# Optimization experiments

Hardware: AMD Instinct MI355X
Metric: run time of the kernel (lower is better)

The kernel has to match this reference:

```python
import jax, jax.numpy as jnp
from jax import lax
import numpy as np

B = 262144
CLASSES = 11


def setup_inputs() -> dict:
    key = jax.random.key(0)
    ks = jax.random.split(key, 8)
    exponents = jax.random.randint(ks[0], (B, 16), 0, CLASSES, dtype=jnp.int32)
    conv0_w = jax.random.normal(ks[1], (4, 12, 1, 2), jnp.float32) * 0.1
    conv0_b = jax.random.normal(ks[2], (4,), jnp.float32) * 0.05
    conv1_w = jax.random.normal(ks[3], (4, 12, 2, 1), jnp.float32) * 0.1
    # xavier-uniform linears, bias filled with 0.01 (as in init_weights)
    lim1 = float(np.sqrt(6.0 / (96 + 256)))
    linear_w = jax.random.uniform(ks[4], (256, 96), jnp.float32, -lim1, lim1)
    linear_b = jnp.full((256,), 0.01, jnp.float32)
    lim2 = float(np.sqrt(6.0 / (256 + 4)))
    out_w = jax.random.uniform(ks[5], (4, 256), jnp.float32, -lim2, lim2)
    out_b = jnp.full((4,), 0.01, jnp.float32)
    return {"exponents": exponents, "conv0_w": conv0_w, "conv0_b": conv0_b,
            "conv1_w": conv1_w, "linear_w": linear_w, "linear_b": linear_b,
            "out_w": out_w, "out_b": out_b}


def _conv(x, w):
    return lax.conv_general_dilated(x, w, (1, 1), 'VALID',
                                    dimension_numbers=('NCHW', 'OIHW', 'NCHW'))


def _forward(exponents, conv0_w, conv0_b, conv1_w, linear_w, linear_b, out_w, out_b):
    e = exponents.reshape(-1, 4, 4)
    # reconstruct board values: 0 tile stays 0, else 2**e
    x = jnp.where(e == 0, 0.0, jnp.exp2(e.astype(jnp.float32)))  # [B,4,4]
    # rotate_normalize: flips chosen from argmax corner (computed BEFORE flipping)
    corners = jnp.stack([x[:, 0, 0], x[:, 0, -1], x[:, -1, 0], x[:, -1, -1]], axis=1)
    ix = jnp.argmax(corners, axis=1)
    flip_v = ix >= 2          # floor(ix/2) == 1
    flip_h = (ix % 2) == 1
    x = jnp.where(flip_v[:, None, None], x[:, ::-1, :], x)
    x = jnp.where(flip_h[:, None, None], x[:, :, ::-1], x)
    # log2 with 0 -> 0, one-hot over 11 classes
    x_log = jnp.log2(x + (x == 0).astype(jnp.float32))
    onehot = jax.nn.one_hot(jnp.round(x_log).astype(jnp.int32), CLASSES,
                            dtype=jnp.float32)          # [B,4,4,11]
    onehot = jnp.transpose(onehot, (0, 3, 1, 2))         # [B,11,4,4]
    mask = onehot.sum(axis=1, keepdims=True)             # channel 0 (all ones)
    feat = jnp.concatenate([mask, onehot], axis=1)       # [B,12,4,4]
    zh = jax.nn.relu(_conv(feat, conv0_w) + conv0_b[None, :, None, None])  # [B,4,4,3]
    zv = jax.nn.relu(_conv(feat, conv1_w))                                  # [B,4,3,4]
    z1 = jnp.concatenate([zh.reshape(-1, 48), zv.reshape(-1, 48)], axis=1)  # [B,96]
    z2 = jax.nn.relu(z1 @ linear_w.T + linear_b)                            # [B,256]
    probs = jax.nn.softmax(z2 @ out_w.T + out_b, axis=1)                    # [B,4]
    # unscramble: vert swaps actions (0,1); horiz swaps actions (2,3)
    perm = jnp.stack([jnp.where(flip_v, 1, 0), jnp.where(flip_v, 0, 1),
                      jnp.where(flip_h, 3, 2), jnp.where(flip_h, 2, 3)], axis=1)
    return jnp.take_along_axis(probs, perm, axis=1)


def reference(exponents, conv0_w, conv0_b, conv1_w, linear_w, linear_b, out_w, out_b):
    return _forward(exponents, conv0_w, conv0_b, conv1_w, linear_w, linear_b, out_w, out_b)
```

## Files before the change

kernel.cpp:

```cpp
#include <hip/hip_runtime.h>

typedef unsigned int  u32;
typedef unsigned short u16;

typedef float    f4  __attribute__((ext_vector_type(4)));
typedef short    bf8 __attribute__((ext_vector_type(8)));
typedef __fp16   h8  __attribute__((ext_vector_type(8)));
typedef __fp16   h2  __attribute__((ext_vector_type(2)));

#define NBLK  256
#define ZSTR  104

__device__ __forceinline__ u32 bfr(float f) {
    union { float f; u32 u; } v; v.f = f;
    return (v.u + 0x8000u) >> 16;
}
__device__ __forceinline__ u32 pk2(float lo, float hi) { return bfr(lo) | (bfr(hi) << 16); }
__device__ __forceinline__ u32 pkh(float lo, float hi) {
    union { h2 h; u32 u; } v; v.h = __builtin_amdgcn_cvt_pkrtz(lo, hi); return v.u;
}
__device__ __forceinline__ u32 pkmax0(u32 x) {
    u32 r; asm("v_pk_max_f16 %0, %1, %2" : "=v"(r) : "v"(x), "v"(0u)); return r;
}
__device__ __forceinline__ u32 nrev(u32 x) {
    return ((x >> 12) & 0xFu) | ((x >> 4) & 0xF0u) | ((x << 4) & 0xF00u) | ((x << 12) & 0xF000u);
}
__device__ __forceinline__ void ds_fence() {
    asm volatile("" ::: "memory");
    __builtin_amdgcn_sched_barrier(0);
}

__device__ __forceinline__ void phase1_fn(const int4 e4, u16* __restrict__ zrow,
                                          const uint2* __restrict__ Th, const uint2* __restrict__ Tv,
                                          const int m, const int qd,
                                          bf8& zb0, bf8& zb1, bf8& zb2, bool& fv, bool& fh)
{
    u32 pkd = (u32)e4.x | ((u32)e4.y << 4) | ((u32)e4.z << 8) | ((u32)e4.w << 12);
    u32 R0 = (u32)__shfl((int)pkd, m);
    u32 R1 = (u32)__shfl((int)pkd, m + 16);
    u32 R2 = (u32)__shfl((int)pkd, m + 32);
    u32 R3 = (u32)__shfl((int)pkd, m + 48);
    u32 c0v = R0 & 15u, c1v = (R0 >> 12) & 15u, c2v = R3 & 15u, c3v = (R3 >> 12) & 15u;
    u32 best = c0v; int ix = 0;
    if (c1v > best) { best = c1v; ix = 1; }
    if (c2v > best) { best = c2v; ix = 2; }
    if (c3v > best) { best = c3v; ix = 3; }
    fv = (ix >= 2); fh = ((ix & 1) != 0);
    u32 F0 = fv ? R3 : R0;
    u32 F1 = fv ? R2 : R1;
    u32 F2 = fv ? R1 : R2;
    u32 F3 = fv ? R0 : R3;
    if (fh) { F0 = nrev(F0); F1 = nrev(F1); F2 = nrev(F2); F3 = nrev(F3); }

    const u32 Fq = (qd == 0) ? F0 : (qd == 1) ? F1 : (qd == 2) ? F2 : F3;
    u32 nbq0 = Fq & 15u, nbq1 = (Fq >> 4) & 15u, nbq2 = (Fq >> 8) & 15u, nbq3 = (Fq >> 12) & 15u;
    u32 nbc0 = (F0 >> (4*qd)) & 15u, nbc1 = (F1 >> (4*qd)) & 15u;
    u32 nbc2 = (F2 >> (4*qd)) & 15u, nbc3 = (F3 >> (4*qd)) & 15u;

    uint2 H0 = Th[nbq0*11u + nbq1];
    uint2 H1 = Th[nbq1*11u + nbq2];
    uint2 H2 = Th[nbq2*11u + nbq3];
    uint2 V0 = Tv[nbc0*11u + nbc1];
    uint2 V1 = Tv[nbc1*11u + nbc2];
    uint2 V2 = Tv[nbc2*11u + nbc3];

    *(uint2*)(zrow + (qd*3 + 0)*4) = H0;
    *(uint2*)(zrow + (qd*3 + 1)*4) = H1;
    *(uint2*)(zrow + (qd*3 + 2)*4) = H2;
    *(uint2*)(zrow + 48 + (0*4 + qd)*4) = V0;
    *(uint2*)(zrow + 48 + (1*4 + qd)*4) = V1;
    *(uint2*)(zrow + 48 + (2*4 + qd)*4) = V2;

    ds_fence();

    zb0 = *(const bf8*)(zrow + qd*8);
    zb1 = *(const bf8*)(zrow + 32 + qd*8);
    zb2 = *(const bf8*)(zrow + 64 + qd*8);

    ds_fence();
}

__launch_bounds__(1024, 4)
__global__ void smartcnn_fused(const int* __restrict__ exps,
                               const float* __restrict__ c0w, const float* __restrict__ c0b,
                               const float* __restrict__ c1w,
                               const float* __restrict__ lw,  const float* __restrict__ lb,
                               const float* __restrict__ ow,  const float* __restrict__ ob,
                               float* __restrict__ out)
{
    __shared__ u16   afL[48 * 512];
    __shared__ uint2 ThA[121];
    __shared__ uint2 TvA[121];
    __shared__ f4    lbL[64];
    __shared__ u32   owL[2048];
    __shared__ u16   z1[256 * ZSTR];

    const int tid  = threadIdx.x;
    const int w    = tid >> 6;
    const int lane = tid & 63;
    const int m    = lane & 15;
    const int qd   = lane >> 4;

    if (tid < 242) {
        const int e = (tid < 121) ? tid : tid - 121;
        const int v1 = e / 11, v2 = e - v1*11;
        float a[4];
        #pragma unroll
        for (int c = 0; c < 4; ++c) {
            if (tid < 121)
                a[c] = fmaxf(c0w[c*24 + 0] + c0w[c*24 + (1+v1)*2 + 0] + c0b[c]
                           + c0w[c*24 + 1] + c0w[c*24 + (1+v2)*2 + 1], 0.f);
            else
                a[c] = fmaxf(c1w[c*24 + 0] + c1w[c*24 + (1+v1)*2 + 0]
                           + c1w[c*24 + 1] + c1w[c*24 + (1+v2)*2 + 1], 0.f);
        }
        uint2 v = make_uint2(pk2(a[0], a[1]), pk2(a[2], a[3]));
        if (tid < 121) ThA[tid] = v; else TvA[tid - 121] = v;
    }
    if (tid < 64) {
        const int T = tid >> 2, q = tid & 3;
        const int tb = ((T & 1) ? 4 : 0) + (T >> 1) * 32;
        lbL[tid] = *(const f4*)(lb + tb + 8 * q);
    }
    #pragma unroll
    for (int v = 0; v < 6; ++v) {
        const int x   = v * 4096 + tid * 4;
        const int fid = x / 96;
        const int ko0 = x - fid * 96;
        const int r   = fid & 63;
        const int T   = ((fid >> 6) << 2) | (((r >> 5) & 1) << 1) | ((r >> 2) & 1);
        const int gm  = (((r >> 3) & 3) << 2) | (r & 3);
        const int side = (ko0 >= 48) ? 48 : 0;
        const int kq0  = ko0 - side;
        const int kp0  = side + (kq0 % 12) * 4 + kq0 / 12;
        const int base = T * 1536 + gm * 8;
        const f4 fv4 = *(const f4*)(lw + x);
        #pragma unroll
        for (int e = 0; e < 4; ++e) {
            const int kp  = kp0 + 4 * e;
            const int idx = base + ((kp >> 5) << 9) + (((kp >> 3) & 3) << 7) + (kp & 7);
            afL[idx] = (u16)bfr(fv4[e]);
        }
    }
    if (tid < 512) {
        const int gl = tid & 63, wc = tid >> 6;
        const int gm = gl & 15, gq = gl >> 4;
        const int cc = wc & 1, ww = wc >> 1;
        uint4 v = make_uint4(0u, 0u, 0u, 0u);
        if (gm < 4) {
            const int n8 = 64*ww + 32*cc + gq*8;
            const float* orow = ow + gm*256 + n8;
            v.x = pkh(orow[0], orow[1]);
            v.y = pkh(orow[2], orow[3]);
            v.z = pkh(orow[4], orow[5]);
            v.w = pkh(orow[6], orow[7]);
        }
        *(uint4*)(&owL[tid * 4]) = v;
    }
    const float4 obv = *(const float4*)ob;
    u16* zrow = &z1[(w*16 + m) * ZSTR];

    __syncthreads();

    const int wbase = blockIdx.x * 1024 + w * 64;
    int4 e4a = *(const int4*)(exps + (size_t)(wbase + m)*16 + qd*4);
    int4 e4b = *(const int4*)(exps + (size_t)(wbase + 16 + m)*16 + qd*4);

    #pragma unroll 1
    for (int si = 0; si < 2; ++si) {
        bf8 za0, za1, za2, zc0, zc1, zc2;
        bool fva, fha, fvb, fhb;
        phase1_fn(e4a, zrow, &ThA[0], &TvA[0], m, qd, za0, za1, za2, fva, fha);
        phase1_fn(e4b, zrow, &ThA[0], &TvA[0], m, qd, zc0, zc1, zc2, fvb, fhb);

        const int sn = (si < 1) ? si + 1 : si;
        e4a = *(const int4*)(exps + (size_t)(wbase + sn*32 + m)*16 + qd*4);
        e4b = *(const int4*)(exps + (size_t)(wbase + sn*32 + 16 + m)*16 + qd*4);

        f4 pa = {0.f,0.f,0.f,0.f}, pb = {0.f,0.f,0.f,0.f};
        __builtin_amdgcn_s_setprio(1);
        #pragma unroll 1
        for (int c = 0; c < 8; ++c) {
            const u16* ap = &afL[c*3072 + lane*8];
            bf8 a00 = *(const bf8*)(ap);
            bf8 a01 = *(const bf8*)(ap + 512);
            bf8 a02 = *(const bf8*)(ap + 1024);
            bf8 a10 = *(const bf8*)(ap + 1536);
            bf8 a11 = *(const bf8*)(ap + 2048);
            bf8 a12 = *(const bf8*)(ap + 2560);
            f4 lb0 = lbL[c*8 + qd];
            f4 lb1 = lbL[c*8 + 4 + qd];
            union { u32 u[4]; h8 v; } au;
            uint4 owt = *(const uint4*)(&owL[c*256 + lane*4]);
            au.u[0] = owt.x; au.u[1] = owt.y; au.u[2] = owt.z; au.u[3] = owt.w;

            f4 x0 = __builtin_amdgcn_mfma_f32_16x16x32_bf16(a00, za0, lb0, 0, 0, 0);
            x0     = __builtin_amdgcn_mfma_f32_16x16x32_bf16(a01, za1, x0, 0, 0, 0);
            x0     = __builtin_amdgcn_mfma_f32_16x16x32_bf16(a02, za2, x0, 0, 0, 0);
            f4 x1 = __builtin_amdgcn_mfma_f32_16x16x32_bf16(a10, za0, lb1, 0, 0, 0);
            x1     = __builtin_amdgcn_mfma_f32_16x16x32_bf16(a11, za1, x1, 0, 0, 0);
            x1     = __builtin_amdgcn_mfma_f32_16x16x32_bf16(a12, za2, x1, 0, 0, 0);
            union { u32 u[4]; h8 v; } bu;
            bu.u[0] = pkmax0(pkh(x0[0], x0[1]));
            bu.u[1] = pkmax0(pkh(x0[2], x0[3]));
            bu.u[2] = pkmax0(pkh(x1[0], x1[1]));
            bu.u[3] = pkmax0(pkh(x1[2], x1[3]));
            pa = __builtin_amdgcn_mfma_f32_16x16x32_f16(au.v, bu.v, pa, 0, 0, 0);

            f4 y0 = __builtin_amdgcn_mfma_f32_16x16x32_bf16(a00, zc0, lb0, 0, 0, 0);
            y0     = __builtin_amdgcn_mfma_f32_16x16x32_bf16(a01, zc1, y0, 0, 0, 0);
            y0     = __builtin_amdgcn_mfma_f32_16x16x32_bf16(a02, zc2, y0, 0, 0, 0);
            f4 y1 = __builtin_amdgcn_mfma_f32_16x16x32_bf16(a10, zc0, lb1, 0, 0, 0);
            y1     = __builtin_amdgcn_mfma_f32_16x16x32_bf16(a11, zc1, y1, 0, 0, 0);
            y1     = __builtin_amdgcn_mfma_f32_16x16x32_bf16(a12, zc2, y1, 0, 0, 0);
            bu.u[0] = pkmax0(pkh(y0[0], y0[1]));
            bu.u[1] = pkmax0(pkh(y0[2], y0[3]));
            bu.u[2] = pkmax0(pkh(y1[0], y1[1]));
            bu.u[3] = pkmax0(pkh(y1[2], y1[3]));
            pb = __builtin_amdgcn_mfma_f32_16x16x32_f16(au.v, bu.v, pb, 0, 0, 0);
        }
        __builtin_amdgcn_s_setprio(0);

        if (qd == 0) {
            {
                float L0 = pa[0] + obv.x, L1 = pa[1] + obv.y, L2 = pa[2] + obv.z, L3 = pa[3] + obv.w;
                float mx = fmaxf(fmaxf(L0, L1), fmaxf(L2, L3));
                float e0 = __expf(L0-mx), e1 = __expf(L1-mx), e2 = __expf(L2-mx), e3 = __expf(L3-mx);
                float inv = __builtin_amdgcn_rcpf(e0 + e1 + e2 + e3);
                float P0 = e0*inv, P1 = e1*inv, P2 = e2*inv, P3 = e3*inv;
                float4 o;
                o.x = fva ? P1 : P0;
                o.y = fva ? P0 : P1;
                o.z = fha ? P3 : P2;
                o.w = fha ? P2 : P3;
                *(float4*)(out + (size_t)(wbase + si*32 + m) * 4) = o;
            }
            {
                float L0 = pb[0] + obv.x, L1 = pb[1] + obv.y, L2 = pb[2] + obv.z, L3 = pb[3] + obv.w;
                float mx = fmaxf(fmaxf(L0, L1), fmaxf(L2, L3));
                float e0 = __expf(L0-mx), e1 = __expf(L1-mx), e2 = __expf(L2-mx), e3 = __expf(L3-mx);
                float inv = __builtin_amdgcn_rcpf(e0 + e1 + e2 + e3);
                float P0 = e0*inv, P1 = e1*inv, P2 = e2*inv, P3 = e3*inv;
                float4 o;
                o.x = fvb ? P1 : P0;
                o.y = fvb ? P0 : P1;
                o.z = fhb ? P3 : P2;
                o.w = fhb ? P2 : P3;
                *(float4*)(out + (size_t)(wbase + si*32 + 16 + m) * 4) = o;
            }
        }
    }
}

extern "C" void kernel_launch(void* const* d_in, const int* in_sizes, int n_in,
                              void* d_out, int out_size, void* d_ws, size_t ws_size,
                              hipStream_t stream) {
    const int*   exps = (const int*)  d_in[0];
    const float* c0w  = (const float*)d_in[1];
    const float* c0b  = (const float*)d_in[2];
    const float* c1w  = (const float*)d_in[3];
    const float* lw   = (const float*)d_in[4];
    const float* lbv  = (const float*)d_in[5];
    const float* oww  = (const float*)d_in[6];
    const float* obv  = (const float*)d_in[7];
    (void)d_ws; (void)ws_size;
    smartcnn_fused<<<NBLK, 1024, 0, stream>>>(exps, c0w, c0b, c1w, lw, lbv, oww, obv, (float*)d_out);
}
```

Before: 89.34 us.

## Process four 16-row groups per pass so weight LDS loads are shared

The outer two-iteration loop is removed. All four 16-row input groups are now run through phase 1 up front, and a single 8-chunk loop runs the MFMA chain for all four groups. Each chunk's A-fragment, bias and output-weight LDS reads are therefore reused across four groups instead of two, which halves the weight loads per row and gives more independent MFMA chains for latency hiding. The cost is higher register pressure from twelve live bf8 fragments and four accumulators, plus the loss of the overlap between prefetching the next exponents and the MFMA loop.

```diff
diff --git a/kernel.cpp b/kernel.cpp
--- a/kernel.cpp
+++ b/kernel.cpp
@@ -163,92 +163,89 @@
     __syncthreads();
 
     const int wbase = blockIdx.x * 1024 + w * 64;
-    int4 e4a = *(const int4*)(exps + (size_t)(wbase + m)*16 + qd*4);
-    int4 e4b = *(const int4*)(exps + (size_t)(wbase + 16 + m)*16 + qd*4);
-
+
+    bf8 za0, za1, za2, zb0_, zb1_, zb2_, zc0, zc1, zc2, zd0, zd1, zd2;
+    bool fva, fha, fvb, fhb, fvc, fhc, fvd, fhd;
+    {
+        int4 e4 = *(const int4*)(exps + (size_t)(wbase + m)*16 + qd*4);
+        phase1_fn(e4, zrow, &ThA[0], &TvA[0], m, qd, za0, za1, za2, fva, fha);
+    }
+    {
+        int4 e4 = *(const int4*)(exps + (size_t)(wbase + 16 + m)*16 + qd*4);
+        phase1_fn(e4, zrow, &ThA[0], &TvA[0], m, qd, zb0_, zb1_, zb2_, fvb, fhb);
+    }
+    {
+        int4 e4 = *(const int4*)(exps + (size_t)(wbase + 32 + m)*16 + qd*4);
+        phase1_fn(e4, zrow, &ThA[0], &TvA[0], m, qd, zc0, zc1, zc2, fvc, fhc);
+    }
+    {
+        int4 e4 = *(const int4*)(exps + (size_t)(wbase + 48 + m)*16 + qd*4);
+        phase1_fn(e4, zrow, &ThA[0], &TvA[0], m, qd, zd0, zd1, zd2, fvd, fhd);
+    }
+
+    f4 pa = {0.f,0.f,0.f,0.f}, pb = {0.f,0.f,0.f,0.f};
+    f4 pc = {0.f,0.f,0.f,0.f}, pd = {0.f,0.f,0.f,0.f};
+    __builtin_amdgcn_s_setprio(1);
     #pragma unroll 1
-    for (int si = 0; si < 2; ++si) {
-        bf8 za0, za1, za2, zc0, zc1, zc2;
-        bool fva, fha, fvb, fhb;
-        phase1_fn(e4a, zrow, &ThA[0], &TvA[0], m, qd, za0, za1, za2, fva, fha);
-        phase1_fn(e4b, zrow, &ThA[0], &TvA[0], m, qd, zc0, zc1, zc2, fvb, fhb);
-
-        const int sn = (si < 1) ? si + 1 : si;
-        e4a = *(const int4*)(exps + (size_t)(wbase + sn*32 + m)*16 + qd*4);
-        e4b = *(const int4*)(exps + (size_t)(wbase + sn*32 + 16 + m)*16 + qd*4);
-
-        f4 pa = {0.f,0.f,0.f,0.f}, pb = {0.f,0.f,0.f,0.f};
-        __builtin_amdgcn_s_setprio(1);
-        #pragma unroll 1
-        for (int c = 0; c < 8; ++c) {
-            const u16* ap = &afL[c*3072 + lane*8];
-            bf8 a00 = *(const bf8*)(ap);
-            bf8 a01 = *(const bf8*)(ap + 512);
-            bf8 a02 = *(const bf8*)(ap + 1024);
-            bf8 a10 = *(const bf8*)(ap + 1536);
-            bf8 a11 = *(const bf8*)(ap + 2048);
-            bf8 a12 = *(const bf8*)(ap + 2560);
-            f4 lb0 = lbL[c*8 + qd];
-            f4 lb1 = lbL[c*8 + 4 + qd];
-            union { u32 u[4]; h8 v; } au;
-            uint4 owt = *(const uint4*)(&owL[c*256 + lane*4]);
-            au.u[0] = owt.x; au.u[1] = owt.y; au.u[2] = owt.z; au.u[3] = owt.w;
-
-            f4 x0 = __builtin_amdgcn_mfma_f32_16x16x32_bf16(a00, za0, lb0, 0, 0, 0);
-            x0     = __builtin_amdgcn_mfma_f32_16x16x32_bf16(a01, za1, x0, 0, 0, 0);
-            x0     = __builtin_amdgcn_mfma_f32_16x16x32_bf16(a02, za2, x0, 0, 0, 0);
-            f4 x1 = __builtin_amdgcn_mfma_f32_16x16x32_bf16(a10, za0, lb1, 0, 0, 0);
-            x1     = __builtin_amdgcn_mfma_f32_16x16x32_bf16(a11, za1, x1, 0, 0, 0);
-            x1     = __builtin_amdgcn_mfma_f32_16x16x32_bf16(a12, za2, x1, 0, 0, 0);
-            union { u32 u[4]; h8 v; } bu;
-            bu.u[0] = pkmax0(pkh(x0[0], x0[1]));
-            bu.u[1] = pkmax0(pkh(x0[2], x0[3]));
-            bu.u[2] = pkmax0(pkh(x1[0], x1[1]));
-            bu.u[3] = pkmax0(pkh(x1[2], x1[3]));
-            pa = __builtin_amdgcn_mfma_f32_16x16x32_f16(au.v, bu.v, pa, 0, 0, 0);
-
-            f4 y0 = __builtin_amdgcn_mfma_f32_16x16x32_bf16(a00, zc0, lb0, 0, 0, 0);
-            y0     = __builtin_amdgcn_mfma_f32_16x16x32_bf16(a01, zc1, y0, 0, 0, 0);
-            y0     = __builtin_amdgcn_mfma_f32_16x16x32_bf16(a02, zc2, y0, 0, 0, 0);
-            f4 y1 = __builtin_amdgcn_mfma_f32_16x16x32_bf16(a10, zc0, lb1, 0, 0, 0);
-            y1     = __builtin_amdgcn_mfma_f32_16x16x32_bf16(a11, zc1, y1, 0, 0, 0);
-            y1     = __builtin_amdgcn_mfma_f32_16x16x32_bf16(a12, zc2, y1, 0, 0, 0);
-            bu.u[0] = pkmax0(pkh(y0[0], y0[1]));
-            bu.u[1] = pkmax0(pkh(y0[2], y0[3]));
-            bu.u[2] = pkmax0(pkh(y1[0], y1[1]));
-            bu.u[3] = pkmax0(pkh(y1[2], y1[3]));
-            pb = __builtin_amdgcn_mfma_f32_16x16x32_f16(au.v, bu.v, pb, 0, 0, 0);
-        }
-        __builtin_amdgcn_s_setprio(0);
-
-        if (qd == 0) {
-            {
-                float L0 = pa[0] + obv.x, L1 = pa[1] + obv.y, L2 = pa[2] + obv.z, L3 = pa[3] + obv.w;
-                float mx = fmaxf(fmaxf(L0, L1), fmaxf(L2, L3));
-                float e0 = __expf(L0-mx), e1 = __expf(L1-mx), e2 = __expf(L2-mx), e3 = __expf(L3-mx);
-                float inv = __builtin_amdgcn_rcpf(e0 + e1 + e2 + e3);
-                float P0 = e0*inv, P1 = e1*inv, P2 = e2*inv, P3 = e3*inv;
-                float4 o;
-                o.x = fva ? P1 : P0;
-                o.y = fva ? P0 : P1;
-                o.z = fha ? P3 : P2;
-                o.w = fha ? P2 : P3;
-                *(float4*)(out + (size_t)(wbase + si*32 + m) * 4) = o;
-            }
-            {
-                float L0 = pb[0] + obv.x, L1 = pb[1] + obv.y, L2 = pb[2] + obv.z, L3 = pb[3] + obv.w;
-                float mx = fmaxf(fmaxf(L0, L1), fmaxf(L2, L3));
-                float e0 = __expf(L0-mx), e1 = __expf(L1-mx), e2 = __expf(L2-mx), e3 = __expf(L3-mx);
-                float inv = __builtin_amdgcn_rcpf(e0 + e1 + e2 + e3);
-                float P0 = e0*inv, P1 = e1*inv, P2 = e2*inv, P3 = e3*inv;
-                float4 o;
-                o.x = fvb ? P1 : P0;
-                o.y = fvb ? P0 : P1;
-                o.z = fhb ? P3 : P2;
-                o.w = fhb ? P2 : P3;
-                *(float4*)(out + (size_t)(wbase + si*32 + 16 + m) * 4) = o;
-            }
-        }
+    for (int c = 0; c < 8; ++c) {
+        const u16* ap = &afL[c*3072 + lane*8];
+        bf8 a00 = *(const bf8*)(ap);
+        bf8 a01 = *(const bf8*)(ap + 512);
+        bf8 a02 = *(const bf8*)(ap + 1024);
+        bf8 a10 = *(const bf8*)(ap + 1536);
+        bf8 a11 = *(const bf8*)(ap + 2048);
+        bf8 a12 = *(const bf8*)(ap + 2560);
+        f4 lb0 = lbL[c*8 + qd];
+        f4 lb1 = lbL[c*8 + 4 + qd];
+        union { u32 u[4]; h8 v; } au;
+        uint4 owt = *(const uint4*)(&owL[c*256 + lane*4]);
+        au.u[0] = owt.x; au.u[1] = owt.y; au.u[2] = owt.z; au.u[3] = owt.w;
+
+        #define GRP(Z0, Z1, Z2, PG)                                                        \
+        {                                                                                  \
+            f4 x0 = __builtin_amdgcn_mfma_f32_16x16x32_bf16(a00, Z0, lb0, 0, 0, 0);        \
+            x0     = __builtin_amdgcn_mfma_f32_16x16x32_bf16(a01, Z1, x0, 0, 0, 0);        \
+            x0     = __builtin_amdgcn_mfma_f32_16x16x32_bf16(a02, Z2, x0, 0, 0, 0);        \
+            f4 x1 = __builtin_amdgcn_mfma_f32_16x16x32_bf16(a10, Z0, lb1, 0, 0, 0);        \
+            x1     = __builtin_amdgcn_mfma_f32_16x16x32_bf16(a11, Z1, x1, 0, 0, 0);        \
+            x1     = __builtin_amdgcn_mfma_f32_16x16x32_bf16(a12, Z2, x1, 0, 0, 0);        \
+            union { u32 u[4]; h8 v; } bu;                                                  \
+            bu.u[0] = pkmax0(pkh(x0[0], x0[1]));                                           \
+            bu.u[1] = pkmax0(pkh(x0[2], x0[3]));                                           \
+            bu.u[2] = pkmax0(pkh(x1[0], x1[1]));                                           \
+            bu.u[3] = pkmax0(pkh(x1[2], x1[3]));                                           \
+            PG = __builtin_amdgcn_mfma_f32_16x16x32_f16(au.v, bu.v, PG, 0, 0, 0);          \
+        }
+        GRP(za0,  za1,  za2,  pa)
+        GRP(zb0_, zb1_, zb2_, pb)
+        GRP(zc0,  zc1,  zc2,  pc)
+        GRP(zd0,  zd1,  zd2,  pd)
+        #undef GRP
+    }
+    __builtin_amdgcn_s_setprio(0);
+
+    if (qd == 0) {
+        #define EPI(PG, FV, FH, G)                                                         \
+        {                                                                                  \
+            float L0 = PG[0] + obv.x, L1 = PG[1] + obv.y;                                  \
+            float L2 = PG[2] + obv.z, L3 = PG[3] + obv.w;                                  \
+            float mx = fmaxf(fmaxf(L0, L1), fmaxf(L2, L3));                                \
+            float e0 = __expf(L0-mx), e1 = __expf(L1-mx);                                  \
+            float e2 = __expf(L2-mx), e3 = __expf(L3-mx);                                  \
+            float inv = __builtin_amdgcn_rcpf(e0 + e1 + e2 + e3);                          \
+            float P0 = e0*inv, P1 = e1*inv, P2 = e2*inv, P3 = e3*inv;                      \
+            float4 o;                                                                      \
+            o.x = (FV) ? P1 : P0;                                                          \
+            o.y = (FV) ? P0 : P1;                                                          \
+            o.z = (FH) ? P3 : P2;                                                          \
+            o.w = (FH) ? P2 : P3;                                                          \
+            *(float4*)(out + (size_t)(wbase + (G)*16 + m) * 4) = o;                        \
+        }
+        EPI(pa, fva, fha, 0)
+        EPI(pb, fvb, fhb, 1)
+        EPI(pc, fvc, fhc, 2)
+        EPI(pd, fvd, fhd, 3)
+        #undef EPI
     }
 }
 
```

Result: no change. 88.95 us (-0.4%).
